# Kernel tuning notes

Hardware: AMD Instinct MI355X
Metric: run time of the kernel (lower is better)

Reference implementation:

```python
import jax, jax.numpy as jnp
import numpy as np

N = 50000
E = 600000
P = 100000
IN_FEATS = 128
HIDDEN = 128


def _glorot(key, shape):
    fan_in, fan_out = shape[0], shape[1]
    lim = np.sqrt(6.0 / (fan_in + fan_out)).astype(np.float32)
    return jax.random.uniform(key, shape, jnp.float32, -lim, lim)


def setup_inputs() -> dict:
    key = jax.random.key(0)
    ks = jax.random.split(key, 20)
    inp = {
        "x": jax.random.normal(ks[0], (N, IN_FEATS), jnp.float32),
        "edge_src": jax.random.randint(ks[1], (E,), 0, N, jnp.int32),
        "edge_dst": jax.random.randint(ks[2], (E,), 0, N, jnp.int32),
        "pos_src": jax.random.randint(ks[3], (P,), 0, N, jnp.int32),
        "pos_dst": jax.random.randint(ks[4], (P,), 0, N, jnp.int32),
        "neg_src": jax.random.randint(ks[5], (P,), 0, N, jnp.int32),
        "neg_dst": jax.random.randint(ks[6], (P,), 0, N, jnp.int32),
        # SAGEConv layer 1 (in_feats -> hidden)
        "Ws1": _glorot(ks[7], (IN_FEATS, HIDDEN)),
        "Wn1": _glorot(ks[8], (IN_FEATS, HIDDEN)),
        "b1": jnp.zeros((HIDDEN,), jnp.float32),
        # SAGEConv layer 2 (hidden -> hidden)
        "Ws2": _glorot(ks[9], (HIDDEN, HIDDEN)),
        "Wn2": _glorot(ks[10], (HIDDEN, HIDDEN)),
        "b2": jnp.zeros((HIDDEN,), jnp.float32),
        # EdgeDecoder MLP: Linear-ReLU-Linear-ReLU-Linear(->1)
        "Wd1": _glorot(ks[11], (HIDDEN, HIDDEN)),
        "bd1": jnp.zeros((HIDDEN,), jnp.float32),
        "Wd2": _glorot(ks[12], (HIDDEN, HIDDEN)),
        "bd2": jnp.zeros((HIDDEN,), jnp.float32),
        "Wd3": _glorot(ks[13], (HIDDEN, 1)),
        "bd3": jnp.zeros((1,), jnp.float32),
    }
    return inp


def _sage_conv(h, src, dst, Ws, Wn, b):
    # mean aggregation over incoming neighbors, then fc_self + fc_neigh + bias
    msg = h[src]                                             # [E, d]
    agg = jax.ops.segment_sum(msg, dst, num_segments=N)      # [N, d]
    deg = jax.ops.segment_sum(jnp.ones((src.shape[0],), h.dtype), dst,
                              num_segments=N)
    mean = agg / jnp.maximum(deg, 1.0)[:, None]
    return h @ Ws + mean @ Wn + b


def _decode(h, src, dst, Wd1, bd1, Wd2, bd2, Wd3, bd3):
    z = h[src] * h[dst]                                      # [P, d]
    z = jax.nn.relu(z @ Wd1 + bd1)
    z = jax.nn.relu(z @ Wd2 + bd2)
    return z @ Wd3 + bd3                                     # [P, 1]


def reference(x, edge_src, edge_dst, pos_src, pos_dst, neg_src, neg_dst,
              Ws1, Wn1, b1, Ws2, Wn2, b2, Wd1, bd1, Wd2, bd2, Wd3, bd3):
    h = jax.nn.relu(_sage_conv(x, edge_src, edge_dst, Ws1, Wn1, b1))
    h = _sage_conv(h, edge_src, edge_dst, Ws2, Wn2, b2)  # last layer: no act
    h_pos = _decode(h, pos_src, pos_dst, Wd1, bd1, Wd2, bd2, Wd3, bd3)
    h_neg = _decode(h, neg_src, neg_dst, Wd1, bd1, Wd2, bd2, Wd3, bd3)
    return (h_pos, h_neg)
```

## Files before the change

### kernel.cpp

```cpp
#include <hip/hip_runtime.h>
#include <hip/hip_bf16.h>

#define N_NODES 50000
#define N_EDGES 600000
#define N_PAIRS 100000

typedef __attribute__((ext_vector_type(8))) short bf16x8;
typedef __attribute__((ext_vector_type(4))) float f32x4;

__device__ inline unsigned short f2b(float f) {
    unsigned u = __float_as_uint(f);
    unsigned r = u + 0x7fff + ((u >> 16) & 1);
    return (unsigned short)(r >> 16);
}
__device__ inline float b2f(unsigned short h) {
    return __uint_as_float(((unsigned)h) << 16);
}

__global__ void k_prep(const float* __restrict__ x, unsigned short* __restrict__ xb16,
                       const int* __restrict__ edge_dst, int* __restrict__ deg,
                       const float* __restrict__ Ws1, const float* __restrict__ Wn1,
                       const float* __restrict__ Ws2, const float* __restrict__ Wn2,
                       const float* __restrict__ Wd1, const float* __restrict__ Wd2,
                       unsigned short* __restrict__ WT1, unsigned short* __restrict__ WT2,
                       unsigned short* __restrict__ WdT1, unsigned short* __restrict__ WdT2) {
    int idx = blockIdx.x * blockDim.x + threadIdx.x;
    if (idx < N_EDGES) atomicAdd(&deg[edge_dst[idx]], 1);
    if (idx < 98304) {
        int id = idx;
        if (id < 32768) {
            int j = id & 7, g = id >> 3;
            int lane = g & 63, t = g >> 6;
            int ct = t & 7, kb = t >> 3;
            int k = kb * 32 + (lane >> 4) * 8 + j, n = ct * 16 + (lane & 15);
            float v = (k < 128) ? Ws1[k * 128 + n] : Wn1[(k - 128) * 128 + n];
            WT1[id] = f2b(v);
        } else if (id < 65536) {
            int r = id - 32768;
            int j = r & 7, g = r >> 3;
            int lane = g & 63, t = g >> 6;
            int ct = t & 7, kb = t >> 3;
            int k = kb * 32 + (lane >> 4) * 8 + j, n = ct * 16 + (lane & 15);
            float v = (k < 128) ? Ws2[k * 128 + n] : Wn2[(k - 128) * 128 + n];
            WT2[r] = f2b(v);
        } else if (id < 81920) {
            int r = id - 65536;
            int j = r & 7, g = r >> 3;
            int lane = g & 63, t = g >> 6;
            int ct = t & 7, kb = t >> 3;
            int k = kb * 32 + (lane >> 4) * 8 + j, n = ct * 16 + (lane & 15);
            WdT1[r] = f2b(Wd1[k * 128 + n]);
        } else {
            int r = id - 81920;
            int j = r & 7, g = r >> 3;
            int lane = g & 63, t = g >> 6;
            int ct = t & 7, kb = t >> 3;
            int k = kb * 32 + (lane >> 4) * 8 + j, n = ct * 16 + (lane & 15);
            WdT2[r] = f2b(Wd2[k * 128 + n]);
        }
    }
    if (idx >= N_NODES * 32) return;
    int row = idx >> 5, c4 = (idx & 31) * 4;
    float4 v = *(const float4*)(x + row * 128 + c4);
    unsigned lo = (unsigned)f2b(v.x) | ((unsigned)f2b(v.y) << 16);
    unsigned hi = (unsigned)f2b(v.z) | ((unsigned)f2b(v.w) << 16);
    uint2 o; o.x = lo; o.y = hi;
    *(uint2*)(xb16 + row * 128 + c4) = o;
}

__global__ void k_scan1(const int* __restrict__ deg, int* __restrict__ row_ptr,
                        int* __restrict__ bsum, int n) {
    __shared__ int tmp[1024];
    int i = blockIdx.x * 1024 + threadIdx.x;
    int d = (i < n) ? deg[i] : 0;
    tmp[threadIdx.x] = d;
    __syncthreads();
    int run = d;
    for (int off = 1; off < 1024; off <<= 1) {
        int t = (threadIdx.x >= off) ? tmp[threadIdx.x - off] : 0;
        __syncthreads();
        run += t;
        tmp[threadIdx.x] = run;
        __syncthreads();
    }
    if (i < n) row_ptr[i] = run - d;
    if (threadIdx.x == 1023) bsum[blockIdx.x] = run;
}

__global__ void k_add(int* __restrict__ row_ptr, int* __restrict__ cursor,
                      const int* __restrict__ bsum, int n) {
    __shared__ int prefix;
    if (threadIdx.x == 0) {
        int acc = 0;
        for (int j = 0; j < (int)blockIdx.x; j++) acc += bsum[j];
        prefix = acc;
    }
    __syncthreads();
    int i = blockIdx.x * 1024 + threadIdx.x;
    if (i < n) {
        int v = row_ptr[i] + prefix;
        row_ptr[i] = v;
        cursor[i] = v;
    }
    if (i == 0) row_ptr[n] = N_EDGES;
}

__global__ void k_scatter(const int* __restrict__ src, const int* __restrict__ dst,
                          int* __restrict__ cursor, int* __restrict__ colA) {
    int e = blockIdx.x * blockDim.x + threadIdx.x;
    if (e < N_EDGES) {
        int d = dst[e];
        int slot = atomicAdd(&cursor[d], 1);
        colA[slot] = src[e];
    }
}

__global__ __launch_bounds__(512) void k_fused(const unsigned short* __restrict__ selfB,
                                               const int* __restrict__ row_ptr,
                                               const int* __restrict__ colA,
                                               const unsigned short* __restrict__ BT,
                                               const float* __restrict__ bias,
                                               unsigned short* __restrict__ Hout,
                                               int M, int relu) {
    __shared__ unsigned short mt[128][136];
    const int tid = threadIdx.x;
    const int wv = tid >> 6, lane = tid & 63;
    const int q = lane >> 4, ql = lane & 15;
    const int r0 = blockIdx.x * 128;

#pragma unroll 1
    for (int round = 0; round < 4; round++) {
        int i = round * 32 + wv * 4 + q;
        int w = r0 + i;
        bool act = (w < M);
        int wc = min(w, M - 1);
        int s = row_ptr[wc], e = row_ptr[wc + 1];
        float a[8];
#pragma unroll
        for (int j = 0; j < 8; j++) a[j] = 0.f;
        for (int base = s; base < e; base += 16) {
            int ce = (base + ql < e) ? colA[base + ql] : 0;
            int cnt = min(16, e - base);
            int ei[16];
#pragma unroll
            for (int j = 0; j < 16; j++) {
                int sl = (j < cnt) ? j : (cnt - 1);
                ei[j] = __shfl(ce, (q << 4) + sl, 64);
            }
            uint4 v[16];
#pragma unroll
            for (int j = 0; j < 16; j++)
                v[j] = *(const uint4*)(selfB + (size_t)ei[j] * 128 + ql * 8);
#pragma unroll
            for (int j = 0; j < 16; j += 2) {
                const unsigned* p0 = (const unsigned*)&v[j];
                const unsigned* p1 = (const unsigned*)&v[j + 1];
                if (j + 1 < cnt) {
#pragma unroll
                    for (int t = 0; t < 4; t++) {
                        a[2 * t] += b2f(p0[t] & 0xffff) + b2f(p1[t] & 0xffff);
                        a[2 * t + 1] += b2f(p0[t] >> 16) + b2f(p1[t] >> 16);
                    }
                } else if (j < cnt) {
#pragma unroll
                    for (int t = 0; t < 4; t++) {
                        a[2 * t] += b2f(p0[t] & 0xffff);
                        a[2 * t + 1] += b2f(p0[t] >> 16);
                    }
                }
            }
        }
        float rd = 1.0f / (float)max(e - s, 1);
        uint4 o;
        unsigned* op = (unsigned*)&o;
#pragma unroll
        for (int t = 0; t < 4; t++)
            op[t] = (unsigned)f2b(a[2 * t] * rd) | ((unsigned)f2b(a[2 * t + 1] * rd) << 16);
        if (act) *(uint4*)(&mt[i][ql * 8]) = o;
    }
    __syncthreads();

    const int lr = lane & 15, lq = lane >> 4;
    const int rw0 = r0 + wv * 16;
    const int arow = min(rw0 + lr, M - 1);
    f32x4 acc[8];
    f32x4 zero = {0.f, 0.f, 0.f, 0.f};
#pragma unroll
    for (int ct = 0; ct < 8; ct++) acc[ct] = zero;
#pragma unroll
    for (int kbi = 0; kbi < 8; kbi++) {
        bf16x8 wf[8];
#pragma unroll
        for (int ct = 0; ct < 8; ct++)
            wf[ct] = *(const bf16x8*)(BT + ((size_t)(kbi * 8 + ct) * 64 + lane) * 8);
        bf16x8 af;
        if (kbi < 4) {
            af = *(const bf16x8*)(selfB + (size_t)arow * 128 + kbi * 32 + lq * 8);
        } else {
            af = *(const bf16x8*)(&mt[arow - r0][(kbi - 4) * 32 + lq * 8]);
        }
#pragma unroll
        for (int ct = 0; ct < 8; ct++)
            acc[ct] = __builtin_amdgcn_mfma_f32_16x16x32_bf16(af, wf[ct], acc[ct], 0, 0, 0);
    }
    __syncthreads();
#pragma unroll
    for (int ct = 0; ct < 8; ct++) {
        int colc = ct * 16 + lr;
        float bv = bias[colc];
#pragma unroll
        for (int r = 0; r < 4; r++) {
            float v = acc[ct][r] + bv;
            if (relu) v = fmaxf(v, 0.f);
            mt[wv * 16 + lq * 4 + r][colc] = f2b(v);
        }
    }
    __syncthreads();
    int rr = tid >> 2, cc = tid & 3;
    int grow = r0 + rr;
    if (grow < M) {
#pragma unroll
        for (int c = 0; c < 4; c++) {
            int so = c * 32 + cc * 8;
            *(uint4*)(Hout + (size_t)grow * 128 + so) = *(const uint4*)(&mt[rr][so]);
        }
    }
}

__global__ __launch_bounds__(512, 2) void k_mlp(const unsigned short* __restrict__ h2b,
                                                const int* __restrict__ pos_src,
                                                const int* __restrict__ pos_dst,
                                                const int* __restrict__ neg_src,
                                                const int* __restrict__ neg_dst,
                                                const unsigned short* __restrict__ WdT1,
                                                const unsigned short* __restrict__ WdT2,
                                                const float* __restrict__ bd1,
                                                const float* __restrict__ bd2,
                                                const float* __restrict__ Wd3,
                                                const float* __restrict__ bd3,
                                                float* __restrict__ out, int P2) {
    __shared__ unsigned short wds[32768];
    __shared__ unsigned short t1[8][32][136];
    const int tid = threadIdx.x;
    {
        const uint4* s1 = (const uint4*)WdT1;
        const uint4* s2 = (const uint4*)WdT2;
        uint4* d = (uint4*)wds;
#pragma unroll
        for (int i = 0; i < 4; i++) d[tid + i * 512] = s1[tid + i * 512];
#pragma unroll
        for (int i = 0; i < 4; i++) d[2048 + tid + i * 512] = s2[tid + i * 512];
    }
    __syncthreads();
    const unsigned short* wd1 = wds;
    const unsigned short* wd2 = wds + 16384;
    const int wv = tid >> 6;
    const int lane = tid & 63, lr = lane & 15, lq = lane >> 4;
    const int nw = gridDim.x << 3;
    const int nt = P2 >> 5;

    uint4 z[16];
    auto ISSUE = [&](int tile) {
        const int row0 = tile * 32;
        int p0 = min(row0 + lr, P2 - 1);
        int p1 = min(row0 + 16 + lr, P2 - 1);
        int s0i = (p0 < N_PAIRS) ? pos_src[p0] : neg_src[p0 - N_PAIRS];
        int d0i = (p0 < N_PAIRS) ? pos_dst[p0] : neg_dst[p0 - N_PAIRS];
        int s1i = (p1 < N_PAIRS) ? pos_src[p1] : neg_src[p1 - N_PAIRS];
        int d1i = (p1 < N_PAIRS) ? pos_dst[p1] : neg_dst[p1 - N_PAIRS];
#pragma unroll
        for (int kb = 0; kb < 4; kb++) {
            int ka = kb * 32 + lq * 8;
            z[kb]      = *(const uint4*)(h2b + (size_t)s0i * 128 + ka);
            z[4 + kb]  = *(const uint4*)(h2b + (size_t)d0i * 128 + ka);
            z[8 + kb]  = *(const uint4*)(h2b + (size_t)s1i * 128 + ka);
            z[12 + kb] = *(const uint4*)(h2b + (size_t)d1i * 128 + ka);
        }
    };

    bf16x8 af0[4], af1[4];
    auto REPACK = [&]() {
#pragma unroll
        for (int kb = 0; kb < 4; kb++) {
            unsigned r0v[4], r1v[4];
            const unsigned* a0p = (const unsigned*)&z[kb];
            const unsigned* b0p = (const unsigned*)&z[4 + kb];
            const unsigned* a1p = (const unsigned*)&z[8 + kb];
            const unsigned* b1p = (const unsigned*)&z[12 + kb];
#pragma unroll
            for (int j = 0; j < 4; j++) {
                unsigned short lo0 = f2b(b2f(a0p[j] & 0xffff) * b2f(b0p[j] & 0xffff));
                unsigned short hi0 = f2b(b2f(a0p[j] >> 16) * b2f(b0p[j] >> 16));
                r0v[j] = (unsigned)lo0 | ((unsigned)hi0 << 16);
                unsigned short lo1 = f2b(b2f(a1p[j] & 0xffff) * b2f(b1p[j] & 0xffff));
                unsigned short hi1 = f2b(b2f(a1p[j] >> 16) * b2f(b1p[j] >> 16));
                r1v[j] = (unsigned)lo1 | ((unsigned)hi1 << 16);
            }
            af0[kb] = *(const bf16x8*)r0v;
            af1[kb] = *(const bf16x8*)r1v;
        }
    };

    auto COMPUTE_REST = [&](int tile) {
        const int row0 = tile * 32;
        f32x4 zero = {0.f, 0.f, 0.f, 0.f};
        f32x4 acc[2][8];
#pragma unroll
        for (int m = 0; m < 2; m++)
#pragma unroll
            for (int ct = 0; ct < 8; ct++) acc[m][ct] = zero;
#pragma unroll
        for (int kb = 0; kb < 4; kb++) {
            bf16x8 wf[8];
#pragma unroll
            for (int ct = 0; ct < 8; ct++)
                wf[ct] = *(const bf16x8*)(wd1 + ((kb * 8 + ct) * 64 + lane) * 8);
#pragma unroll
            for (int ct = 0; ct < 8; ct++) {
                acc[0][ct] = __builtin_amdgcn_mfma_f32_16x16x32_bf16(af0[kb], wf[ct], acc[0][ct], 0, 0, 0);
                acc[1][ct] = __builtin_amdgcn_mfma_f32_16x16x32_bf16(af1[kb], wf[ct], acc[1][ct], 0, 0, 0);
            }
        }
#pragma unroll
        for (int m = 0; m < 2; m++)
#pragma unroll
            for (int ct = 0; ct < 8; ct++) {
                int colc = ct * 16 + lr;
                float bv = bd1[colc];
#pragma unroll
                for (int r = 0; r < 4; r++) {
                    float v = fmaxf(acc[m][ct][r] + bv, 0.f);
                    t1[wv][m * 16 + lq * 4 + r][colc] = f2b(v);
                }
            }
        asm volatile("s_waitcnt lgkmcnt(0)" ::: "memory");
#pragma unroll
        for (int m = 0; m < 2; m++)
#pragma unroll
            for (int ct = 0; ct < 8; ct++) acc[m][ct] = zero;
#pragma unroll
        for (int kb = 0; kb < 4; kb++) {
            int ka = kb * 32 + lq * 8;
            bf16x8 wf[8];
#pragma unroll
            for (int ct = 0; ct < 8; ct++)
                wf[ct] = *(const bf16x8*)(wd2 + ((kb * 8 + ct) * 64 + lane) * 8);
            bf16x8 bf0 = *(const bf16x8*)(&t1[wv][lr][ka]);
            bf16x8 bf1 = *(const bf16x8*)(&t1[wv][16 + lr][ka]);
#pragma unroll
            for (int ct = 0; ct < 8; ct++) {
                acc[0][ct] = __builtin_amdgcn_mfma_f32_16x16x32_bf16(bf0, wf[ct], acc[0][ct], 0, 0, 0);
                acc[1][ct] = __builtin_amdgcn_mfma_f32_16x16x32_bf16(bf1, wf[ct], acc[1][ct], 0, 0, 0);
            }
        }
        float sc[2][4] = {{0.f, 0.f, 0.f, 0.f}, {0.f, 0.f, 0.f, 0.f}};
#pragma unroll
        for (int ct = 0; ct < 8; ct++) {
            int colc = ct * 16 + lr;
            float bv = bd2[colc];
            float w3 = Wd3[colc];
#pragma unroll
            for (int m = 0; m < 2; m++)
#pragma unroll
                for (int r = 0; r < 4; r++) {
                    float v = fmaxf(acc[m][ct][r] + bv, 0.f);
                    sc[m][r] += v * w3;
                }
        }
#pragma unroll
        for (int mm = 1; mm < 16; mm <<= 1)
#pragma unroll
            for (int m = 0; m < 2; m++)
#pragma unroll
                for (int r = 0; r < 4; r++) sc[m][r] += __shfl_xor(sc[m][r], mm, 64);
        if (lr == 0) {
            float b3 = bd3[0];
#pragma unroll
            for (int m = 0; m < 2; m++)
#pragma unroll
                for (int r = 0; r < 4; r++) {
                    int g = row0 + m * 16 + lq * 4 + r;
                    if (g < P2) out[g] = sc[m][r] + b3;
                }
        }
    };

    int t = blockIdx.x * 8 + wv;
    if (t >= nt) return;
    ISSUE(t);
    while (true) {
        REPACK();
        int tn = t + nw;
        if (tn < nt) ISSUE(tn);
        COMPUTE_REST(t);
        if (tn >= nt) break;
        t = tn;
    }
}

static inline size_t alignup(size_t v) { return (v + 255) & ~(size_t)255; }

extern "C" void kernel_launch(void* const* d_in, const int* in_sizes, int n_in,
                              void* d_out, int out_size, void* d_ws, size_t ws_size,
                              hipStream_t stream) {
    const float* x = (const float*)d_in[0];
    const int* edge_src = (const int*)d_in[1];
    const int* edge_dst = (const int*)d_in[2];
    const int* pos_src = (const int*)d_in[3];
    const int* pos_dst = (const int*)d_in[4];
    const int* neg_src = (const int*)d_in[5];
    const int* neg_dst = (const int*)d_in[6];
    const float* Ws1 = (const float*)d_in[7];
    const float* Wn1 = (const float*)d_in[8];
    const float* b1 = (const float*)d_in[9];
    const float* Ws2 = (const float*)d_in[10];
    const float* Wn2 = (const float*)d_in[11];
    const float* b2 = (const float*)d_in[12];
    const float* Wd1 = (const float*)d_in[13];
    const float* bd1 = (const float*)d_in[14];
    const float* Wd2 = (const float*)d_in[15];
    const float* bd2 = (const float*)d_in[16];
    const float* Wd3 = (const float*)d_in[17];
    const float* bd3 = (const float*)d_in[18];
    float* out = (float*)d_out;

    char* p = (char*)d_ws;
    int* deg = (int*)p;            p += alignup(N_NODES * 4);
    int* row_ptr = (int*)p;        p += alignup((N_NODES + 1) * 4);
    int* cursor = (int*)p;         p += alignup(N_NODES * 4);
    int* bsum = (int*)p;           p += alignup(64 * 4);
    int* colA = (int*)p;           p += alignup(N_EDGES * 4);
    unsigned short* h1 = (unsigned short*)p;  p += alignup((size_t)N_NODES * 128 * 2);
    unsigned short* h2b = (unsigned short*)p; p += alignup((size_t)N_NODES * 128 * 2);
    unsigned short* WT1 = (unsigned short*)p;  p += alignup(32768 * 2);
    unsigned short* WT2 = (unsigned short*)p;  p += alignup(32768 * 2);
    unsigned short* WdT1 = (unsigned short*)p; p += alignup(16384 * 2);
    unsigned short* WdT2 = (unsigned short*)p; p += alignup(16384 * 2);
    unsigned short* xb16 = h2b;

    hipMemsetAsync(deg, 0, N_NODES * 4, stream);

    k_prep<<<(N_NODES * 32 + 255) / 256, 256, 0, stream>>>(
        x, xb16, edge_dst, deg,
        Ws1, Wn1, Ws2, Wn2, Wd1, Wd2, WT1, WT2, WdT1, WdT2);

    int nb1 = (N_NODES + 1023) / 1024;
    k_scan1<<<nb1, 1024, 0, stream>>>(deg, row_ptr, bsum, N_NODES);
    k_add<<<nb1, 1024, 0, stream>>>(row_ptr, cursor, bsum, N_NODES);
    k_scatter<<<(N_EDGES + 255) / 256, 256, 0, stream>>>(edge_src, edge_dst, cursor, colA);

    int nblk = (N_NODES + 127) / 128;

    k_fused<<<nblk, 512, 0, stream>>>(xb16, row_ptr, colA, WT1, b1, h1, N_NODES, 1);
    k_fused<<<nblk, 512, 0, stream>>>(h1, row_ptr, colA, WT2, b2, h2b, N_NODES, 0);

    k_mlp<<<256, 512, 0, stream>>>(h2b, pos_src, pos_dst, neg_src, neg_dst,
                                   WdT1, WdT2, bd1, bd2, Wd3, bd3,
                                   out, N_PAIRS * 2);
}
```

Before: 274.7 us.

## Software-pipeline neighbor gathers and interleave self-term MFMA with aggregation in k_fused

Restructures the fused SAGE kernel so that the row pointers and column indices for all four rounds are loaded up front. The first gather batch for the next row (or next 16-edge chunk) is issued before the current one is consumed, hiding gather latency. The self-feature half of the matmul (kbi 0..3) now runs inside the aggregation loop, overlapping MFMA with memory work, and only the neighbor half remains after the barrier. Launch bounds now request 2 blocks per CU, which caps registers and may cause spills given the extra live state (v[16], acc[8], prefetch arrays).

```diff
diff --git a/kernel.cpp b/kernel.cpp
--- a/kernel.cpp
+++ b/kernel.cpp
@@ -115,42 +115,61 @@
     }
 }
 
-__global__ __launch_bounds__(512) void k_fused(const unsigned short* __restrict__ selfB,
-                                               const int* __restrict__ row_ptr,
-                                               const int* __restrict__ colA,
-                                               const unsigned short* __restrict__ BT,
-                                               const float* __restrict__ bias,
-                                               unsigned short* __restrict__ Hout,
-                                               int M, int relu) {
+__global__ __launch_bounds__(512, 2) void k_fused(const unsigned short* __restrict__ selfB,
+                                                  const int* __restrict__ row_ptr,
+                                                  const int* __restrict__ colA,
+                                                  const unsigned short* __restrict__ BT,
+                                                  const float* __restrict__ bias,
+                                                  unsigned short* __restrict__ Hout,
+                                                  int M, int relu) {
     __shared__ unsigned short mt[128][136];
     const int tid = threadIdx.x;
     const int wv = tid >> 6, lane = tid & 63;
     const int q = lane >> 4, ql = lane & 15;
+    const int lr = lane & 15, lq = lane >> 4;
     const int r0 = blockIdx.x * 128;
+    const int arow = min(r0 + wv * 16 + lr, M - 1);
+
+    f32x4 acc[8];
+    f32x4 zero = {0.f, 0.f, 0.f, 0.f};
+#pragma unroll
+    for (int ct = 0; ct < 8; ct++) acc[ct] = zero;
+
+    int sA[4], eA[4], ceA[4];
+#pragma unroll
+    for (int r = 0; r < 4; r++) {
+        int i = r * 32 + wv * 4 + q;
+        int wc = min(r0 + i, M - 1);
+        sA[r] = row_ptr[wc];
+        eA[r] = row_ptr[wc + 1];
+    }
+#pragma unroll
+    for (int r = 0; r < 4; r++)
+        ceA[r] = (sA[r] + ql < eA[r]) ? colA[sA[r] + ql] : 0;
+
+    uint4 v[16];
+    int ei[16];
+    {
+        int cnt0 = min(16, eA[0] - sA[0]);
+#pragma unroll
+        for (int j = 0; j < 16; j++) {
+            int sl = (j < cnt0) ? j : (cnt0 - 1);
+            ei[j] = __shfl(ceA[0], (q << 4) + sl, 64);
+        }
+#pragma unroll
+        for (int j = 0; j < 16; j++)
+            v[j] = *(const uint4*)(selfB + (size_t)ei[j] * 128 + ql * 8);
+    }
 
 #pragma unroll 1
-    for (int round = 0; round < 4; round++) {
-        int i = round * 32 + wv * 4 + q;
-        int w = r0 + i;
-        bool act = (w < M);
-        int wc = min(w, M - 1);
-        int s = row_ptr[wc], e = row_ptr[wc + 1];
+    for (int r = 0; r < 4; r++) {
         float a[8];
 #pragma unroll
         for (int j = 0; j < 8; j++) a[j] = 0.f;
-        for (int base = s; base < e; base += 16) {
-            int ce = (base + ql < e) ? colA[base + ql] : 0;
+        int s = sA[r], e = eA[r];
+        int base = s;
+        while (true) {
             int cnt = min(16, e - base);
-            int ei[16];
-#pragma unroll
-            for (int j = 0; j < 16; j++) {
-                int sl = (j < cnt) ? j : (cnt - 1);
-                ei[j] = __shfl(ce, (q << 4) + sl, 64);
-            }
-            uint4 v[16];
-#pragma unroll
-            for (int j = 0; j < 16; j++)
-                v[j] = *(const uint4*)(selfB + (size_t)ei[j] * 128 + ql * 8);
 #pragma unroll
             for (int j = 0; j < 16; j += 2) {
                 const unsigned* p0 = (const unsigned*)&v[j];
@@ -169,6 +188,18 @@
                     }
                 }
             }
+            base += 16;
+            if (base >= e) break;
+            int ce = (base + ql < e) ? colA[base + ql] : 0;
+            int cnt2 = min(16, e - base);
+#pragma unroll
+            for (int j = 0; j < 16; j++) {
+                int sl = (j < cnt2) ? j : (cnt2 - 1);
+                ei[j] = __shfl(ce, (q << 4) + sl, 64);
+            }
+#pragma unroll
+            for (int j = 0; j < 16; j++)
+                v[j] = *(const uint4*)(selfB + (size_t)ei[j] * 128 + ql * 8);
         }
         float rd = 1.0f / (float)max(e - s, 1);
         uint4 o;
@@ -176,29 +207,41 @@
 #pragma unroll
         for (int t = 0; t < 4; t++)
             op[t] = (unsigned)f2b(a[2 * t] * rd) | ((unsigned)f2b(a[2 * t + 1] * rd) << 16);
-        if (act) *(uint4*)(&mt[i][ql * 8]) = o;
+        {
+            int i = r * 32 + wv * 4 + q;
+            if (r0 + i < M) *(uint4*)(&mt[i][ql * 8]) = o;
+        }
+        if (r < 3) {
+            int cntn = min(16, eA[r + 1] - sA[r + 1]);
+#pragma unroll
+            for (int j = 0; j < 16; j++) {
+                int sl = (j < cntn) ? j : (cntn - 1);
+                ei[j] = __shfl(ceA[r + 1], (q << 4) + sl, 64);
+            }
+#pragma unroll
+            for (int j = 0; j < 16; j++)
+                v[j] = *(const uint4*)(selfB + (size_t)ei[j] * 128 + ql * 8);
+        }
+        {
+            bf16x8 wfr[8];
+#pragma unroll
+            for (int ct = 0; ct < 8; ct++)
+                wfr[ct] = *(const bf16x8*)(BT + ((size_t)(r * 8 + ct) * 64 + lane) * 8);
+            bf16x8 af = *(const bf16x8*)(selfB + (size_t)arow * 128 + r * 32 + lq * 8);
+#pragma unroll
+            for (int ct = 0; ct < 8; ct++)
+                acc[ct] = __builtin_amdgcn_mfma_f32_16x16x32_bf16(af, wfr[ct], acc[ct], 0, 0, 0);
+        }
     }
     __syncthreads();
 
-    const int lr = lane & 15, lq = lane >> 4;
-    const int rw0 = r0 + wv * 16;
-    const int arow = min(rw0 + lr, M - 1);
-    f32x4 acc[8];
-    f32x4 zero = {0.f, 0.f, 0.f, 0.f};
-#pragma unroll
-    for (int ct = 0; ct < 8; ct++) acc[ct] = zero;
-#pragma unroll
-    for (int kbi = 0; kbi < 8; kbi++) {
+#pragma unroll
+    for (int kbi = 4; kbi < 8; kbi++) {
         bf16x8 wf[8];
 #pragma unroll
         for (int ct = 0; ct < 8; ct++)
             wf[ct] = *(const bf16x8*)(BT + ((size_t)(kbi * 8 + ct) * 64 + lane) * 8);
-        bf16x8 af;
-        if (kbi < 4) {
-            af = *(const bf16x8*)(selfB + (size_t)arow * 128 + kbi * 32 + lq * 8);
-        } else {
-            af = *(const bf16x8*)(&mt[arow - r0][(kbi - 4) * 32 + lq * 8]);
-        }
+        bf16x8 af = *(const bf16x8*)(&mt[arow - r0][(kbi - 4) * 32 + lq * 8]);
 #pragma unroll
         for (int ct = 0; ct < 8; ct++)
             acc[ct] = __builtin_amdgcn_mfma_f32_16x16x32_bf16(af, wf[ct], acc[ct], 0, 0, 0);
@@ -210,9 +253,9 @@
         float bv = bias[colc];
 #pragma unroll
         for (int r = 0; r < 4; r++) {
-            float v = acc[ct][r] + bv;
-            if (relu) v = fmaxf(v, 0.f);
-            mt[wv * 16 + lq * 4 + r][colc] = f2b(v);
+            float v2 = acc[ct][r] + bv;
+            if (relu) v2 = fmaxf(v2, 0.f);
+            mt[wv * 16 + lq * 4 + r][colc] = f2b(v2);
         }
     }
     __syncthreads();
```

After: 300.3 us. 1.09x slower.
